# Kernel tuning notes

Hardware: AMD Instinct MI355X
Metric: run time of the kernel (lower is better)

Reference implementation:

```python
import jax, jax.numpy as jnp
import numpy as np

B, S, D, H, DFF = 2, 2048, 1024, 16, 4096
DK = D // H
EPS = 1e-6

def setup_inputs() -> dict:
    key = jax.random.key(0)
    ks = jax.random.split(key, 12)
    sc = 0.02
    inp = {
        "x": jax.random.normal(ks[0], (B, S, D), jnp.float32),
        "src_mask": jax.random.randint(ks[1], (B, 1, 1, S), 0, 2, jnp.int32),
        "wq": jax.random.normal(ks[2], (D, D), jnp.float32) * sc,
        "bq": jnp.zeros((D,), jnp.float32),
        "wk": jax.random.normal(ks[3], (D, D), jnp.float32) * sc,
        "bk": jnp.zeros((D,), jnp.float32),
        "wv": jax.random.normal(ks[4], (D, D), jnp.float32) * sc,
        "bv": jnp.zeros((D,), jnp.float32),
        "wo": jax.random.normal(ks[5], (D, D), jnp.float32) * sc,
        "bo": jnp.zeros((D,), jnp.float32),
        "w1": jax.random.normal(ks[6], (DFF, D), jnp.float32) * sc,
        "b1": jnp.zeros((DFF,), jnp.float32),
        "w2": jax.random.normal(ks[7], (D, DFF), jnp.float32) * sc,
        "b2": jnp.zeros((D,), jnp.float32),
        "a1": jnp.ones((1,), jnp.float32),
        "be1": jnp.zeros((1,), jnp.float32),
        "a2": jnp.ones((1,), jnp.float32),
        "be2": jnp.zeros((1,), jnp.float32),
    }
    return inp

def layer_norm(x, alpha, beta):
    # custom LN: unbiased std (ddof=1), scalar alpha/beta, divide by (std + eps)
    mean = jnp.mean(x, axis=-1, keepdims=True)
    std = jnp.std(x, axis=-1, keepdims=True, ddof=1)
    return alpha * (x - mean) / (std + EPS) + beta

def mha(x, mask, wq, bq, wk, bk, wv, bv, wo, bo):
    q = (x @ wq.T + bq).reshape(B, S, H, DK).transpose(0, 2, 1, 3)  # [B,H,S,DK]
    k = (x @ wk.T + bk).reshape(B, S, H, DK).transpose(0, 2, 1, 3)
    v = (x @ wv.T + bv).reshape(B, S, H, DK).transpose(0, 2, 1, 3)
    scores = jnp.einsum('bhqd,bhkd->bhqk', q, k) / jnp.sqrt(jnp.float32(DK))
    scores = jnp.where(mask == 0, jnp.float32(-1e9), scores)
    attn = jax.nn.softmax(scores, axis=-1)
    out = jnp.einsum('bhqk,bhkd->bhqd', attn, v)
    out = out.transpose(0, 2, 1, 3).reshape(B, S, D)
    return out @ wo.T + bo

def ffn(x, w1, b1, w2, b2):
    h = jax.nn.relu(x @ w1.T + b1)
    return h @ w2.T + b2

def reference(x, src_mask, wq, bq, wk, bk, wv, bv, wo, bo, w1, b1, w2, b2, a1, be1, a2, be2):
    # pre-norm residual 1: self-attention
    x = x + mha(layer_norm(x, a1, be1), src_mask, wq, bq, wk, bk, wv, bv, wo, bo)
    # pre-norm residual 2: FFN
    x = x + ffn(layer_norm(x, a2, be2), w1, b1, w2, b2)
    return x
```

## Files before the change

kernel.cpp:

```cpp
#include <hip/hip_runtime.h>

#define B_    2
#define S_    2048
#define D_    1024
#define H_    16
#define DK_   64
#define DFF_  4096
#define MROWS (B_*S_)

typedef float f32x4 __attribute__((ext_vector_type(4)));
typedef __bf16 bf16x8 __attribute__((ext_vector_type(8)));

static __device__ __forceinline__ unsigned short f2bf(float f) {
    union { __bf16 h; unsigned short u; } cv;
    cv.h = (__bf16)f;
    return cv.u;
}

static __device__ __forceinline__ void gload16(const unsigned short* g, unsigned short* l) {
    __builtin_amdgcn_global_load_lds((const __attribute__((address_space(1))) void*)g,
                                     (__attribute__((address_space(3))) void*)l, 16, 0, 0);
}

__global__ __launch_bounds__(256) void prep_kernel(
    const float* __restrict__ wq, const float* __restrict__ wk,
    const float* __restrict__ wv, const float* __restrict__ wo,
    const float* __restrict__ w1, const float* __restrict__ w2,
    const float* __restrict__ bq, const float* __restrict__ bk,
    unsigned short* __restrict__ wqkb, unsigned short* __restrict__ wvb,
    unsigned short* __restrict__ wob, unsigned short* __restrict__ w1b,
    unsigned short* __restrict__ w2b, float* __restrict__ bqk) {
    int blk = blockIdx.x;
    if (blk >= 12288) {
        int t0 = threadIdx.x * 8;
        #pragma unroll
        for (int i = 0; i < 8; i++) {
            int j = t0 + i;
            bqk[j] = (j < 1024) ? bq[j] : bk[j - 1024];
        }
        return;
    }
    const float* src; unsigned short* dst; int lb;
    if      (blk < 1024) { src = wq; dst = wqkb;             lb = blk;        }
    else if (blk < 2048) { src = wk; dst = wqkb + (1 << 20); lb = blk - 1024; }
    else if (blk < 3072) { src = wv; dst = wvb;              lb = blk - 2048; }
    else if (blk < 4096) { src = wo; dst = wob;              lb = blk - 3072; }
    else if (blk < 8192) { src = w1; dst = w1b;              lb = blk - 4096; }
    else                 { src = w2; dst = w2b;              lb = blk - 8192; }
    int i4 = lb * 256 + threadIdx.x;
    float4 v = ((const float4*)src)[i4];
    ushort4 o;
    o.x = f2bf(v.x); o.y = f2bf(v.y); o.z = f2bf(v.z); o.w = f2bf(v.w);
    ((ushort4*)dst)[i4] = o;
}

__global__ __launch_bounds__(256) void ln_kernel(const float* __restrict__ x,
                                                 const float* __restrict__ alphap,
                                                 const float* __restrict__ betap,
                                                 unsigned short* __restrict__ out) {
    int row = blockIdx.x;
    int t = threadIdx.x;
    const float* xr = x + (size_t)row * D_;
    float4 v = ((const float4*)xr)[t];
    float s  = v.x + v.y + v.z + v.w;
    float s2 = v.x*v.x + v.y*v.y + v.z*v.z + v.w*v.w;
    #pragma unroll
    for (int o = 1; o < 64; o <<= 1) { s += __shfl_xor(s, o); s2 += __shfl_xor(s2, o); }
    __shared__ float ss[4], ss2[4];
    if ((t & 63) == 0) { ss[t >> 6] = s; ss2[t >> 6] = s2; }
    __syncthreads();
    float S  = ss[0] + ss[1] + ss[2] + ss[3];
    float S2 = ss2[0] + ss2[1] + ss2[2] + ss2[3];
    float mean = S * (1.f / (float)D_);
    float var  = (S2 - S * mean) / (float)(D_ - 1);
    float alpha = alphap[0], beta = betap[0];
    float inv = alpha / (sqrtf(fmaxf(var, 0.f)) + 1e-6f);
    ushort4 o4;
    o4.x = f2bf((v.x - mean) * inv + beta);
    o4.y = f2bf((v.y - mean) * inv + beta);
    o4.z = f2bf((v.z - mean) * inv + beta);
    o4.w = f2bf((v.w - mean) * inv + beta);
    ((ushort4*)(out + (size_t)row * D_))[t] = o4;
}

template<int BN, int EPI, int BIAS_ROW, int QSCALE>
__global__ __launch_bounds__(256) void gemm_bt(const unsigned short* __restrict__ A,
                                               const unsigned short* __restrict__ W,
                                               const float* __restrict__ bias,
                                               const float* __restrict__ resid,
                                               unsigned short* __restrict__ outb,
                                               float* __restrict__ outf,
                                               int M, int N, int K) {
    constexpr int NI = BN / 32;
    __shared__ __align__(16) unsigned short As[128 * 64];
    __shared__ __align__(16) unsigned short Bs[BN * 64];
    const int t = threadIdx.x, lane = t & 63, w = t >> 6;
    const int m0 = blockIdx.y * 128, n0 = blockIdx.x * BN;
    const int wm = (w & 1) * 64;
    const int wn = (BN == 128) ? (w >> 1) * 64 : (w >> 1) * 32;
    const int l15 = lane & 15, l4 = lane >> 4;
    const int ar0 = w * 8 + (lane >> 3);
    const int ac0 = (lane & 7) * 8;

    f32x4 acc[4][NI];
    f32x4 z4 = {0.f, 0.f, 0.f, 0.f};
    #pragma unroll
    for (int i = 0; i < 4; i++)
        #pragma unroll
        for (int j = 0; j < NI; j++) acc[i][j] = z4;

    const unsigned short* Ap = A + (size_t)m0 * K;
    const unsigned short* Wp = W + (size_t)n0 * K;

    for (int k0 = 0; k0 < K; k0 += 64) {
        #pragma unroll
        for (int j = 0; j < 4; j++)
            gload16(Ap + (size_t)(j*32 + ar0) * K + k0 + ac0, &As[(j*4 + w) * 512]);
        #pragma unroll
        for (int j = 0; j < BN/32; j++)
            gload16(Wp + (size_t)(j*32 + ar0) * K + k0 + ac0, &Bs[(j*4 + w) * 512]);
        __syncthreads();

        #pragma unroll
        for (int ks = 0; ks < 2; ks++) {
            bf16x8 af[4], bfr[NI];
            #pragma unroll
            for (int mi = 0; mi < 4; mi++)
                af[mi] = *(const bf16x8*)&As[(wm + mi*16 + l15)*64 + ks*32 + l4*8];
            #pragma unroll
            for (int ni = 0; ni < NI; ni++)
                bfr[ni] = *(const bf16x8*)&Bs[(wn + ni*16 + l15)*64 + ks*32 + l4*8];
            #pragma unroll
            for (int mi = 0; mi < 4; mi++)
                #pragma unroll
                for (int ni = 0; ni < NI; ni++)
                    acc[mi][ni] = __builtin_amdgcn_mfma_f32_16x16x32_bf16(af[mi], bfr[ni], acc[mi][ni], 0, 0, 0);
        }
        __syncthreads();
    }

    #pragma unroll
    for (int mi = 0; mi < 4; mi++) {
        #pragma unroll
        for (int ni = 0; ni < NI; ni++) {
            int gc = n0 + wn + ni*16 + l15;
            float bc = BIAS_ROW ? 0.f : bias[gc];
            #pragma unroll
            for (int j = 0; j < 4; j++) {
                int gr = m0 + wm + mi*16 + 4*l4 + j;
                float val = acc[mi][ni][j] + (BIAS_ROW ? bias[gr] : bc);
                if (EPI == 1) val = fmaxf(val, 0.f);
                if (QSCALE) { if (gc < (N >> 1)) val *= 0.125f; }
                if (EPI == 2) {
                    val += resid[(size_t)gr * N + gc];
                    outf[(size_t)gr * N + gc] = val;
                } else {
                    outb[(size_t)gr * N + gc] = f2bf(val);
                }
            }
        }
    }
}

__global__ __launch_bounds__(256) void attn_kernel(const unsigned short* __restrict__ qk,
                                                   const unsigned short* __restrict__ vt,
                                                   const int* __restrict__ mask,
                                                   unsigned short* __restrict__ out) {
    __shared__ __align__(16) unsigned short Ks[64*64], Vs[64*64], Ps[64*64];
    __shared__ int mS[64];
    const int t = threadIdx.x, lane = t & 63, w = t >> 6;
    const int l15 = lane & 15, l4 = lane >> 4;
    const int bh = blockIdx.y, b = bh >> 4, h = bh & 15;
    const int q0 = blockIdx.x * 64;
    const unsigned short* qb  = qk + ((size_t)(b * S_ + q0)) * 2048 + h * DK_;
    const unsigned short* kb  = qk + ((size_t)(b * S_)) * 2048 + 1024 + h * DK_;
    const unsigned short* vtb = vt + (size_t)(h * DK_) * MROWS + (size_t)b * S_;

    bf16x8 aq[2];
    #pragma unroll
    for (int ks = 0; ks < 2; ks++)
        aq[ks] = *(const bf16x8*)(qb + (size_t)(w*16 + l15) * 2048 + ks*32 + l4*8);

    float m_[4], l_[4];
    f32x4 accd[4];
    f32x4 z4 = {0.f, 0.f, 0.f, 0.f};
    #pragma unroll
    for (int j = 0; j < 4; j++) { m_[j] = -INFINITY; l_[j] = 0.f; }
    #pragma unroll
    for (int dt = 0; dt < 4; dt++) accd[dt] = z4;

    const int r_  = t >> 3, c8_ = (t & 7) * 8;
    const int cs_ = c8_ ^ ((r_ & 7) << 3);
    const int rsw = (l15 & 7) << 3;

    for (int kv0 = 0; kv0 < S_; kv0 += 64) {
        #pragma unroll
        for (int p = 0; p < 2; p++) {
            int r = r_ + p * 32;
            *(uint4*)&Ks[r*64 + cs_] = *(const uint4*)(kb  + (size_t)(kv0 + r) * 2048 + c8_);
            *(uint4*)&Vs[r*64 + cs_] = *(const uint4*)(vtb + (size_t)r * MROWS + kv0 + c8_);
        }
        if (t < 64) mS[t] = mask[(size_t)b * S_ + kv0 + t];
        __syncthreads();

        f32x4 sc[4];
        #pragma unroll
        for (int nt = 0; nt < 4; nt++) sc[nt] = z4;
        #pragma unroll
        for (int nt = 0; nt < 4; nt++)
            #pragma unroll
            for (int ks = 0; ks < 2; ks++) {
                bf16x8 bk8 = *(const bf16x8*)&Ks[(nt*16 + l15)*64 + ((ks*32 + 8*l4) ^ rsw)];
                sc[nt] = __builtin_amdgcn_mfma_f32_16x16x32_bf16(aq[ks], bk8, sc[nt], 0, 0, 0);
            }

        float sv[4][4];
        int mk[4];
        #pragma unroll
        for (int nt = 0; nt < 4; nt++) mk[nt] = mS[nt*16 + l15];
        #pragma unroll
        for (int nt = 0; nt < 4; nt++)
            #pragma unroll
            for (int j = 0; j < 4; j++)
                sv[nt][j] = (mk[nt] == 0) ? -1e9f : sc[nt][j];

        float mx[4];
        #pragma unroll
        for (int j = 0; j < 4; j++) {
            float mxx = fmaxf(fmaxf(sv[0][j], sv[1][j]), fmaxf(sv[2][j], sv[3][j]));
            #pragma unroll
            for (int o = 1; o < 16; o <<= 1) mxx = fmaxf(mxx, __shfl_xor(mxx, o));
            mx[j] = mxx;
        }
        bool upd = (mx[0] > m_[0]) | (mx[1] > m_[1]) | (mx[2] > m_[2]) | (mx[3] > m_[3]);
        if (__any(upd)) {
            #pragma unroll
            for (int j = 0; j < 4; j++) {
                float mn  = fmaxf(m_[j], mx[j]);
                float esc = __expf(m_[j] - mn);
                m_[j] = mn;
                l_[j] *= esc;
                #pragma unroll
                for (int dt = 0; dt < 4; dt++) accd[dt][j] *= esc;
            }
        }
        float rs[4] = {0.f, 0.f, 0.f, 0.f};
        float p[4][4];
        #pragma unroll
        for (int nt = 0; nt < 4; nt++)
            #pragma unroll
            for (int j = 0; j < 4; j++) { p[nt][j] = __expf(sv[nt][j] - m_[j]); rs[j] += p[nt][j]; }
        #pragma unroll
        for (int j = 0; j < 4; j++) {
            #pragma unroll
            for (int o = 1; o < 16; o <<= 1) rs[j] += __shfl_xor(rs[j], o);
            l_[j] += rs[j];
        }

        #pragma unroll
        for (int nt = 0; nt < 4; nt++)
            #pragma unroll
            for (int j = 0; j < 4; j++) {
                int pr = w*16 + 4*l4 + j;
                Ps[pr*64 + ((nt*16 + l15) ^ (((4*l4 + j) & 7) << 3))] = f2bf(p[nt][j]);
            }

        bf16x8 pa[2];
        #pragma unroll
        for (int ks = 0; ks < 2; ks++)
            pa[ks] = *(const bf16x8*)&Ps[(w*16 + l15)*64 + ((ks*32 + 8*l4) ^ rsw)];
        #pragma unroll
        for (int dt = 0; dt < 4; dt++)
            #pragma unroll
            for (int ks = 0; ks < 2; ks++) {
                bf16x8 vv8 = *(const bf16x8*)&Vs[(dt*16 + l15)*64 + ((ks*32 + 8*l4) ^ rsw)];
                accd[dt] = __builtin_amdgcn_mfma_f32_16x16x32_bf16(pa[ks], vv8, accd[dt], 0, 0, 0);
            }
        __syncthreads();
    }

    unsigned short* ob = out + ((size_t)(b * S_ + q0)) * D_ + h * DK_;
    #pragma unroll
    for (int j = 0; j < 4; j++) {
        float inv = 1.f / l_[j];
        int r = w*16 + 4*l4 + j;
        #pragma unroll
        for (int dt = 0; dt < 4; dt++)
            ob[(size_t)r * D_ + dt*16 + l15] = f2bf(accd[dt][j] * inv);
    }
}

extern "C" void kernel_launch(void* const* d_in, const int* in_sizes, int n_in,
                              void* d_out, int out_size, void* d_ws, size_t ws_size,
                              hipStream_t stream) {
    const float* x    = (const float*)d_in[0];
    const int*   mask = (const int*)d_in[1];
    const float* wq = (const float*)d_in[2];
    const float* bq = (const float*)d_in[3];
    const float* wk = (const float*)d_in[4];
    const float* bk = (const float*)d_in[5];
    const float* wv = (const float*)d_in[6];
    const float* bv = (const float*)d_in[7];
    const float* wo = (const float*)d_in[8];
    const float* bo = (const float*)d_in[9];
    const float* w1 = (const float*)d_in[10];
    const float* b1 = (const float*)d_in[11];
    const float* w2 = (const float*)d_in[12];
    const float* b2 = (const float*)d_in[13];
    const float* a1  = (const float*)d_in[14];
    const float* be1 = (const float*)d_in[15];
    const float* a2  = (const float*)d_in[16];
    const float* be2 = (const float*)d_in[17];
    float* out = (float*)d_out;

    char* ws = (char*)d_ws;
    unsigned short* wqkb = (unsigned short*)(ws + (0ull  << 20));
    unsigned short* wvb  = (unsigned short*)(ws + (4ull  << 20));
    unsigned short* wob  = (unsigned short*)(ws + (6ull  << 20));
    unsigned short* w1b  = (unsigned short*)(ws + (8ull  << 20));
    unsigned short* w2b  = (unsigned short*)(ws + (16ull << 20));
    unsigned short* xn   = (unsigned short*)(ws + (24ull << 20));
    unsigned short* qkb  = (unsigned short*)(ws + (32ull << 20));
    unsigned short* vtb  = (unsigned short*)(ws + (48ull << 20));
    float*          bqk  = (float*)         (ws + (60ull << 20));
    unsigned short* hh   = qkb;
    float*          x1   = (float*)(ws + (64ull << 20));

    dim3 blk(256);

    prep_kernel<<<12289, blk, 0, stream>>>(wq, wk, wv, wo, w1, w2, bq, bk,
                                           wqkb, wvb, wob, w1b, w2b, bqk);

    ln_kernel<<<MROWS, blk, 0, stream>>>(x, a1, be1, xn);

    dim3 gqk(2048/128, MROWS/128);
    gemm_bt<128,0,0,1><<<gqk, blk, 0, stream>>>(xn, wqkb, bqk, nullptr, qkb, nullptr, MROWS, 2048, D_);

    dim3 gvt(MROWS/64, D_/128);
    gemm_bt<64,0,1,0><<<gvt, blk, 0, stream>>>(wvb, xn, bv, nullptr, vtb, nullptr, D_, MROWS, D_);

    dim3 ga(S_/64, B_*H_);
    attn_kernel<<<ga, blk, 0, stream>>>(qkb, vtb, mask, xn);

    dim3 go(D_/64, MROWS/128);
    gemm_bt<64,2,0,0><<<go, blk, 0, stream>>>(xn, wob, bo, x, nullptr, x1, MROWS, D_, D_);

    ln_kernel<<<MROWS, blk, 0, stream>>>(x1, a2, be2, xn);

    dim3 gf1(DFF_/128, MROWS/128);
    gemm_bt<128,1,0,0><<<gf1, blk, 0, stream>>>(xn, w1b, b1, nullptr, hh, nullptr, MROWS, DFF_, D_);

    gemm_bt<64,2,0,0><<<go, blk, 0, stream>>>(hh, w2b, b2, x1, nullptr, out, MROWS, D_, DFF_);
}
```

Before: 447.3 us.

## Transpose QK MFMA operands for per-lane softmax rows and swizzle GEMM workgroups

The attention kernel swaps the MFMA operands so each lane holds scores for a single query row. This shrinks the row max and row sum reductions from four 4-step shuffle trees to two shuffles, and lets P be written to LDS as packed 8-byte stores. The mask is converted once into an additive float bias, so the per-element compare and select becomes an add. The GEMM also remaps block IDs round-robin across 8 groups, aiming to improve L2 locality on the multi-XCD MI355X at the cost of some index arithmetic.

```diff
diff --git a/kernel.cpp b/kernel.cpp
--- a/kernel.cpp
+++ b/kernel.cpp
@@ -95,7 +95,11 @@
     __shared__ __align__(16) unsigned short As[128 * 64];
     __shared__ __align__(16) unsigned short Bs[BN * 64];
     const int t = threadIdx.x, lane = t & 63, w = t >> 6;
-    const int m0 = blockIdx.y * 128, n0 = blockIdx.x * BN;
+    const int nwg  = gridDim.x * gridDim.y;
+    const int orig = blockIdx.y * gridDim.x + blockIdx.x;
+    const int wg   = (orig & 7) * (nwg >> 3) + (orig >> 3);
+    const int bx   = wg % gridDim.x, by = wg / gridDim.x;
+    const int m0 = by * 128, n0 = bx * BN;
     const int wm = (w & 1) * 64;
     const int wn = (BN == 128) ? (w >> 1) * 64 : (w >> 1) * 32;
     const int l15 = lane & 15, l4 = lane >> 4;
@@ -167,7 +171,7 @@
                                                    const int* __restrict__ mask,
                                                    unsigned short* __restrict__ out) {
     __shared__ __align__(16) unsigned short Ks[64*64], Vs[64*64], Ps[64*64];
-    __shared__ int mS[64];
+    __shared__ float mF[64];
     const int t = threadIdx.x, lane = t & 63, w = t >> 6;
     const int l15 = lane & 15, l4 = lane >> 4;
     const int bh = blockIdx.y, b = bh >> 4, h = bh & 15;
@@ -181,11 +185,9 @@
     for (int ks = 0; ks < 2; ks++)
         aq[ks] = *(const bf16x8*)(qb + (size_t)(w*16 + l15) * 2048 + ks*32 + l4*8);
 
-    float m_[4], l_[4];
+    float m_ = -INFINITY, l_ = 0.f;
     f32x4 accd[4];
     f32x4 z4 = {0.f, 0.f, 0.f, 0.f};
-    #pragma unroll
-    for (int j = 0; j < 4; j++) { m_[j] = -INFINITY; l_[j] = 0.f; }
     #pragma unroll
     for (int dt = 0; dt < 4; dt++) accd[dt] = z4;
 
@@ -195,12 +197,12 @@
 
     for (int kv0 = 0; kv0 < S_; kv0 += 64) {
         #pragma unroll
-        for (int p = 0; p < 2; p++) {
-            int r = r_ + p * 32;
+        for (int p2 = 0; p2 < 2; p2++) {
+            int r = r_ + p2 * 32;
             *(uint4*)&Ks[r*64 + cs_] = *(const uint4*)(kb  + (size_t)(kv0 + r) * 2048 + c8_);
             *(uint4*)&Vs[r*64 + cs_] = *(const uint4*)(vtb + (size_t)r * MROWS + kv0 + c8_);
         }
-        if (t < 64) mS[t] = mask[(size_t)b * S_ + kv0 + t];
+        if (t < 64) mF[t] = (mask[(size_t)b * S_ + kv0 + t] == 0) ? -1e9f : 0.f;
         __syncthreads();
 
         f32x4 sc[4];
@@ -210,60 +212,59 @@
         for (int nt = 0; nt < 4; nt++)
             #pragma unroll
             for (int ks = 0; ks < 2; ks++) {
-                bf16x8 bk8 = *(const bf16x8*)&Ks[(nt*16 + l15)*64 + ((ks*32 + 8*l4) ^ rsw)];
-                sc[nt] = __builtin_amdgcn_mfma_f32_16x16x32_bf16(aq[ks], bk8, sc[nt], 0, 0, 0);
+                bf16x8 kf = *(const bf16x8*)&Ks[(nt*16 + l15)*64 + ((ks*32 + 8*l4) ^ rsw)];
+                sc[nt] = __builtin_amdgcn_mfma_f32_16x16x32_bf16(kf, aq[ks], sc[nt], 0, 0, 0);
             }
 
         float sv[4][4];
-        int mk[4];
-        #pragma unroll
-        for (int nt = 0; nt < 4; nt++) mk[nt] = mS[nt*16 + l15];
+        #pragma unroll
+        for (int nt = 0; nt < 4; nt++) {
+            float4 ma = *(const float4*)&mF[nt*16 + 4*l4];
+            sv[nt][0] = sc[nt][0] + ma.x;
+            sv[nt][1] = sc[nt][1] + ma.y;
+            sv[nt][2] = sc[nt][2] + ma.z;
+            sv[nt][3] = sc[nt][3] + ma.w;
+        }
+
+        float mt = fmaxf(fmaxf(fmaxf(sv[0][0], sv[0][1]), fmaxf(sv[0][2], sv[0][3])),
+                         fmaxf(fmaxf(sv[1][0], sv[1][1]), fmaxf(sv[1][2], sv[1][3])));
+        mt = fmaxf(mt, fmaxf(fmaxf(fmaxf(sv[2][0], sv[2][1]), fmaxf(sv[2][2], sv[2][3])),
+                             fmaxf(fmaxf(sv[3][0], sv[3][1]), fmaxf(sv[3][2], sv[3][3]))));
+        mt = fmaxf(mt, __shfl_xor(mt, 16));
+        mt = fmaxf(mt, __shfl_xor(mt, 32));
+
+        if (__any(mt > m_)) {
+            float mn  = fmaxf(m_, mt);
+            float esc = __expf(m_ - mn);
+            m_ = mn;
+            l_ *= esc;
+            float ea[4];
+            #pragma unroll
+            for (int j = 0; j < 4; j++) ea[j] = __shfl(esc, 4*l4 + j);
+            #pragma unroll
+            for (int dt = 0; dt < 4; dt++)
+                #pragma unroll
+                for (int j = 0; j < 4; j++) accd[dt][j] *= ea[j];
+        }
+
+        float p[4][4];
+        float rsum = 0.f;
         #pragma unroll
         for (int nt = 0; nt < 4; nt++)
             #pragma unroll
-            for (int j = 0; j < 4; j++)
-                sv[nt][j] = (mk[nt] == 0) ? -1e9f : sc[nt][j];
-
-        float mx[4];
-        #pragma unroll
-        for (int j = 0; j < 4; j++) {
-            float mxx = fmaxf(fmaxf(sv[0][j], sv[1][j]), fmaxf(sv[2][j], sv[3][j]));
-            #pragma unroll
-            for (int o = 1; o < 16; o <<= 1) mxx = fmaxf(mxx, __shfl_xor(mxx, o));
-            mx[j] = mxx;
-        }
-        bool upd = (mx[0] > m_[0]) | (mx[1] > m_[1]) | (mx[2] > m_[2]) | (mx[3] > m_[3]);
-        if (__any(upd)) {
-            #pragma unroll
-            for (int j = 0; j < 4; j++) {
-                float mn  = fmaxf(m_[j], mx[j]);
-                float esc = __expf(m_[j] - mn);
-                m_[j] = mn;
-                l_[j] *= esc;
-                #pragma unroll
-                for (int dt = 0; dt < 4; dt++) accd[dt][j] *= esc;
-            }
-        }
-        float rs[4] = {0.f, 0.f, 0.f, 0.f};
-        float p[4][4];
-        #pragma unroll
-        for (int nt = 0; nt < 4; nt++)
-            #pragma unroll
-            for (int j = 0; j < 4; j++) { p[nt][j] = __expf(sv[nt][j] - m_[j]); rs[j] += p[nt][j]; }
-        #pragma unroll
-        for (int j = 0; j < 4; j++) {
-            #pragma unroll
-            for (int o = 1; o < 16; o <<= 1) rs[j] += __shfl_xor(rs[j], o);
-            l_[j] += rs[j];
-        }
-
-        #pragma unroll
-        for (int nt = 0; nt < 4; nt++)
-            #pragma unroll
-            for (int j = 0; j < 4; j++) {
-                int pr = w*16 + 4*l4 + j;
-                Ps[pr*64 + ((nt*16 + l15) ^ (((4*l4 + j) & 7) << 3))] = f2bf(p[nt][j]);
-            }
+            for (int j = 0; j < 4; j++) { p[nt][j] = __expf(sv[nt][j] - m_); rsum += p[nt][j]; }
+        rsum += __shfl_xor(rsum, 16);
+        rsum += __shfl_xor(rsum, 32);
+        l_ += rsum;
+
+        #pragma unroll
+        for (int nt = 0; nt < 4; nt++) {
+            uint2 w2;
+            w2.x = (unsigned)f2bf(p[nt][0]) | ((unsigned)f2bf(p[nt][1]) << 16);
+            w2.y = (unsigned)f2bf(p[nt][2]) | ((unsigned)f2bf(p[nt][3]) << 16);
+            int key0 = nt*16 + 4*l4;
+            *(uint2*)&Ps[(w*16 + l15)*64 + (key0 ^ rsw)] = w2;
+        }
 
         bf16x8 pa[2];
         #pragma unroll
@@ -279,14 +280,17 @@
         __syncthreads();
     }
 
+    float inv = 1.f / l_;
+    float ia[4];
+    #pragma unroll
+    for (int j = 0; j < 4; j++) ia[j] = __shfl(inv, 4*l4 + j);
     unsigned short* ob = out + ((size_t)(b * S_ + q0)) * D_ + h * DK_;
     #pragma unroll
     for (int j = 0; j < 4; j++) {
-        float inv = 1.f / l_[j];
         int r = w*16 + 4*l4 + j;
         #pragma unroll
         for (int dt = 0; dt < 4; dt++)
-            ob[(size_t)r * D_ + dt*16 + l15] = f2bf(accd[dt][j] * inv);
+            ob[(size_t)r * D_ + dt*16 + l15] = f2bf(accd[dt][j] * ia[j]);
     }
 }
 
```

New measurement: 417.0 us. 6.8% less time.
